# Kernel tuning notes

Hardware: AMD Instinct MI355X
Metric: run time of the kernel (lower is better)

The kernel has to match this reference:

```python
import jax, jax.numpy as jnp
import numpy as np

B, N, DIM, H = 2, 2048, 1024, 16
D = DIM // H

def setup_inputs() -> dict:
    key = jax.random.key(0)
    k1, k2 = jax.random.split(key)
    x = jax.random.normal(k1, (B, N, DIM), dtype=jnp.float32)
    w_qkv = jax.random.normal(k2, (3 * DIM, DIM), dtype=jnp.float32) * (DIM ** -0.5)
    return {"x": x, "w_qkv": w_qkv}

def reference(x, w_qkv):
    b, n, dim = x.shape
    h, d = H, dim // H
    # fused QKV projection: torch Linear computes x @ W.T
    qkv = jnp.einsum('bnd,ed->bne', x, w_qkv)  # [B, N, 3*dim]
    q, k, v = jnp.split(qkv, 3, axis=-1)
    to_heads = lambda t: t.reshape(b, n, h, d).transpose(0, 2, 1, 3)  # [B, H, N, D]
    q, k, v = to_heads(q), to_heads(k), to_heads(v)
    dots = jnp.einsum('bhid,bhjd->bhij', q, k) * (d ** -0.5)  # [B, H, N, N]
    attn = jax.nn.softmax(dots, axis=-1)
    out = jnp.einsum('bhij,bhjd->bhid', attn, v)  # [B, H, N, D]
    # faithful to original: (B,H,N,D) -> (B,N,H,D) -> (B, N*H, D)
    return out.transpose(0, 2, 1, 3).reshape(b, n * h, d)
```

## Files before the change

### kernel.cpp

```cpp
#include <hip/hip_runtime.h>

typedef unsigned short u16;
typedef __bf16 bf16x8 __attribute__((ext_vector_type(8)));
typedef float f32x4 __attribute__((ext_vector_type(4)));

#define BATCH 2
#define NSEQ  2048
#define DIMN  1024
#define NH    16
#define DH    64
#define M_    (BATCH * NSEQ)
#define E_    (3 * DIMN)
#define K_    DIMN
#define QKV_BYTES ((size_t)M_ * E_ * sizeof(u16))
#define XB_ELEMS  ((size_t)M_ * K_)
#define WB_ELEMS  ((size_t)E_ * K_)
#define VT_BYTES  ((size_t)BATCH * NH * DH * NSEQ * sizeof(u16))
#define NEED2     (QKV_BYTES + (XB_ELEMS + WB_ELEMS) * sizeof(u16))
#define NEED3     (NEED2 + VT_BYTES)

__device__ __forceinline__ u16 f2bf(float f) {
  union { float f; unsigned u; } v; v.f = f;
  unsigned r = v.u + 0x7fffu + ((v.u >> 16) & 1u);
  return (u16)(r >> 16);
}
__device__ __forceinline__ uint4 pack8(const float4 a, const float4 b) {
  union { u16 h[8]; uint4 q; } p;
  p.h[0] = f2bf(a.x); p.h[1] = f2bf(a.y); p.h[2] = f2bf(a.z); p.h[3] = f2bf(a.w);
  p.h[4] = f2bf(b.x); p.h[5] = f2bf(b.y); p.h[6] = f2bf(b.z); p.h[7] = f2bf(b.w);
  return p.q;
}
__device__ __forceinline__ void async16(const void* g, void* lds) {
  __builtin_amdgcn_global_load_lds(
      (const __attribute__((address_space(1))) void*)g,
      (__attribute__((address_space(3))) void*)lds, 16, 0, 0);
}
__device__ __forceinline__ unsigned cvtpk_bf16(float lo, float hi) {
  unsigned r;
  asm("v_cvt_pk_bf16_f32 %0, %1, %2" : "=v"(r) : "v"(lo), "v"(hi));
  return r;
}

__global__ __launch_bounds__(256, 4)
void convert_bf16(const float* __restrict__ X, const float* __restrict__ W,
                  u16* __restrict__ Xb, u16* __restrict__ Wb) {
  const size_t nx = XB_ELEMS / 8, nw = WB_ELEMS / 8;
  const size_t stride = (size_t)gridDim.x * blockDim.x;
  for (size_t i = blockIdx.x * blockDim.x + threadIdx.x; i < nx; i += stride) {
    const float4 a = *(const float4*)&X[i * 8];
    const float4 b = *(const float4*)&X[i * 8 + 4];
    *(uint4*)&Xb[i * 8] = pack8(a, b);
  }
  for (size_t i = blockIdx.x * blockDim.x + threadIdx.x; i < nw; i += stride) {
    const float4 a = *(const float4*)&W[i * 8];
    const float4 b = *(const float4*)&W[i * 8 + 4];
    *(uint4*)&Wb[i * 8] = pack8(a, b);
  }
}

__global__ __launch_bounds__(256, 2)
void qkv_gemm_a(const u16* __restrict__ Xb, const u16* __restrict__ Wb,
                u16* __restrict__ QKV, u16* __restrict__ VTg) {
  __shared__ __align__(16) u16 As[128 * 64];
  __shared__ __align__(16) u16 Bs[128 * 64];
  const int tid  = threadIdx.x;
  const int wave = tid >> 6, lane = tid & 63;
  const int m0 = blockIdx.x * 128;
  const int n0 = blockIdx.y * 128;
  const int wm = (wave >> 1) * 64;
  const int wn = (wave & 1) * 64;
  const int lcol = lane & 15, lrow = lane >> 4;
  const int lr8 = lane >> 3;
  const int slog = (lane & 7) ^ lr8;

  f32x4 acc[4][4] = {};

  for (int k0 = 0; k0 < K_; k0 += 64) {
    __syncthreads();
    #pragma unroll
    for (int i = 0; i < 4; ++i) {
      const int g = wave * 4 + i;
      const int r = g * 8 + lr8;
      async16(Xb + (size_t)(m0 + r) * K_ + k0 + slog * 8, &As[g * 512]);
      async16(Wb + (size_t)(n0 + r) * K_ + k0 + slog * 8, &Bs[g * 512]);
    }
    __syncthreads();
    #pragma unroll
    for (int ks = 0; ks < 64; ks += 32) {
      const int segl = (ks >> 3) + lrow;
      bf16x8 af[4], bfr[4];
      #pragma unroll
      for (int i = 0; i < 4; ++i) {
        const int r = wm + lcol + 16 * i;
        af[i] = *(const bf16x8*)&As[r * 64 + ((segl ^ (r & 7)) * 8)];
      }
      #pragma unroll
      for (int j = 0; j < 4; ++j) {
        const int r = wn + lcol + 16 * j;
        bfr[j] = *(const bf16x8*)&Bs[r * 64 + ((segl ^ (r & 7)) * 8)];
      }
      #pragma unroll
      for (int i = 0; i < 4; ++i)
        #pragma unroll
        for (int j = 0; j < 4; ++j)
          acc[i][j] = __builtin_amdgcn_mfma_f32_16x16x32_bf16(
              af[i], bfr[j], acc[i][j], 0, 0, 0);
    }
  }

  if (n0 >= 2 * DIMN) {
    #pragma unroll
    for (int i = 0; i < 4; ++i)
      #pragma unroll
      for (int j = 0; j < 4; ++j) {
        const int gm = m0 + wm + 16 * i + lrow * 4;
        const int bb = gm >> 11, n = gm & (NSEQ - 1);
        const int f = (n0 - 2 * DIMN) + wn + 16 * j + lcol;
        const int h = f >> 6, dd = f & (DH - 1);
        union { u16 h4[4]; uint2 q; } pk;
        #pragma unroll
        for (int r = 0; r < 4; ++r) pk.h4[r] = f2bf(acc[i][j][r]);
        *(uint2*)&VTg[(((size_t)bb * NH + h) * DH + dd) * NSEQ + n] = pk.q;
      }
  } else {
    #pragma unroll
    for (int i = 0; i < 4; ++i)
      #pragma unroll
      for (int j = 0; j < 4; ++j)
        #pragma unroll
        for (int r = 0; r < 4; ++r) {
          const int gm = m0 + wm + 16 * i + lrow * 4 + r;
          const int gn = n0 + wn + 16 * j + lcol;
          QKV[(size_t)gm * E_ + gn] = f2bf(acc[i][j][r]);
        }
  }
}

__global__ __launch_bounds__(256, 2)
void qkv_gemm_f(const float* __restrict__ X, const float* __restrict__ W,
                u16* __restrict__ QKV) {
  __shared__ __align__(16) u16 As[128 * 64];
  __shared__ __align__(16) u16 Bs[128 * 64];
  const int tid  = threadIdx.x;
  const int wave = tid >> 6, lane = tid & 63;
  const int m0 = blockIdx.x * 128, n0 = blockIdx.y * 128;
  const int wm = (wave >> 1) * 64, wn = (wave & 1) * 64;
  const int lcol = lane & 15, lrow = lane >> 4;
  f32x4 acc[4][4] = {};
  for (int k0 = 0; k0 < K_; k0 += 64) {
    __syncthreads();
    #pragma unroll
    for (int p = 0; p < 4; ++p) {
      const int linear = p * 256 + tid;
      const int r = linear >> 3, s = linear & 7;
      const float4 a0 = *(const float4*)&X[(size_t)(m0 + r) * K_ + k0 + s * 8];
      const float4 a1 = *(const float4*)&X[(size_t)(m0 + r) * K_ + k0 + s * 8 + 4];
      const float4 b0 = *(const float4*)&W[(size_t)(n0 + r) * K_ + k0 + s * 8];
      const float4 b1 = *(const float4*)&W[(size_t)(n0 + r) * K_ + k0 + s * 8 + 4];
      const int ph = (s ^ (r & 7)) * 8;
      *(uint4*)&As[r * 64 + ph] = pack8(a0, a1);
      *(uint4*)&Bs[r * 64 + ph] = pack8(b0, b1);
    }
    __syncthreads();
    #pragma unroll
    for (int ks = 0; ks < 64; ks += 32) {
      const int segl = (ks >> 3) + lrow;
      bf16x8 af[4], bfr[4];
      #pragma unroll
      for (int i = 0; i < 4; ++i) {
        const int r = wm + lcol + 16 * i;
        af[i] = *(const bf16x8*)&As[r * 64 + ((segl ^ (r & 7)) * 8)];
      }
      #pragma unroll
      for (int j = 0; j < 4; ++j) {
        const int r = wn + lcol + 16 * j;
        bfr[j] = *(const bf16x8*)&Bs[r * 64 + ((segl ^ (r & 7)) * 8)];
      }
      #pragma unroll
      for (int i = 0; i < 4; ++i)
        #pragma unroll
        for (int j = 0; j < 4; ++j)
          acc[i][j] = __builtin_amdgcn_mfma_f32_16x16x32_bf16(
              af[i], bfr[j], acc[i][j], 0, 0, 0);
    }
  }
  #pragma unroll
  for (int i = 0; i < 4; ++i)
    #pragma unroll
    for (int j = 0; j < 4; ++j)
      #pragma unroll
      for (int r = 0; r < 4; ++r) {
        const int gm = m0 + wm + 16 * i + lrow * 4 + r;
        const int gn = n0 + wn + 16 * j + lcol;
        QKV[(size_t)gm * E_ + gn] = f2bf(acc[i][j][r]);
      }
}

__global__ __launch_bounds__(256, 2)
void attn2(const u16* __restrict__ QKV, const u16* __restrict__ VTg,
           float* __restrict__ Out) {
  __shared__ __align__(16) u16 Ks[64 * 72];
  __shared__ __align__(16) u16 Vs[64 * 72];

  const int tid = threadIdx.x, wave = tid >> 6, lane = tid & 63;
  const int b = blockIdx.x >> 4, h = blockIdx.x & 15;
  const int i0 = blockIdx.y * 128;
  const int lcol = lane & 15, lrow = lane >> 4;
  const size_t base = (size_t)b * NSEQ;
  const int qoff = h * DH, koff = DIMN + h * DH;
  const size_t vbh = ((size_t)b * NH + h) * DH;
  const int sr = tid >> 3;
  const int sg = tid & 7;

  bf16x8 ones;
  #pragma unroll
  for (int t = 0; t < 8; ++t) ones[t] = (__bf16)1.0f;

  bf16x8 aq[2][2];
  #pragma unroll
  for (int qi = 0; qi < 2; ++qi)
    #pragma unroll
    for (int ksi = 0; ksi < 2; ++ksi) {
      const int row = i0 + wave * 32 + qi * 16 + lcol;
      aq[qi][ksi] = *(const bf16x8*)&QKV[(base + row) * E_ + qoff +
                                         (ksi * 4 + lrow) * 8];
    }

  uint4 kreg[2], vreg[2];
  #pragma unroll
  for (int p = 0; p < 2; ++p) {
    const int row = p * 32 + sr;
    kreg[p] = *(const uint4*)&QKV[(base + row) * E_ + koff + sg * 8];
    vreg[p] = *(const uint4*)&VTg[(vbh + row) * NSEQ + sg * 8];
  }

  f32x4 o[2][4] = {};
  f32x4 lacc[2] = {};

  for (int j0 = 0; j0 < NSEQ; j0 += 64) {
    __syncthreads();
    #pragma unroll
    for (int p = 0; p < 2; ++p) {
      const int row = p * 32 + sr;
      *(uint4*)&Ks[row * 72 + sg * 8] = kreg[p];
      *(uint4*)&Vs[row * 72 + sg * 8] = vreg[p];
    }
    __syncthreads();

    if (j0 + 64 < NSEQ) {
      #pragma unroll
      for (int p = 0; p < 2; ++p) {
        const int row = p * 32 + sr;
        kreg[p] = *(const uint4*)&QKV[(base + j0 + 64 + row) * E_ + koff + sg * 8];
        vreg[p] = *(const uint4*)&VTg[(vbh + row) * NSEQ + j0 + 64 + sg * 8];
      }
    }

    f32x4 s2[2][4] = {};
    #pragma unroll
    for (int ksi = 0; ksi < 2; ++ksi) {
      const int seg = ksi * 4 + lrow;
      #pragma unroll
      for (int jt = 0; jt < 4; ++jt) {
        const bf16x8 bk = *(const bf16x8*)&Ks[(jt * 16 + lcol) * 72 + seg * 8];
        #pragma unroll
        for (int qi = 0; qi < 2; ++qi)
          s2[qi][jt] = __builtin_amdgcn_mfma_f32_16x16x32_bf16(
              bk, aq[qi][ksi], s2[qi][jt], 0, 0, 0);
      }
    }

    unsigned apw[2][2][4];
    #pragma unroll
    for (int qi = 0; qi < 2; ++qi) {
      unsigned dw[4][2];
      #pragma unroll
      for (int jt = 0; jt < 4; ++jt) {
        float p[4];
        #pragma unroll
        for (int r = 0; r < 4; ++r)
          p[r] = exp2f(fmaf(s2[qi][jt][r], 0.180336880f, -17.3123405f));
        dw[jt][0] = cvtpk_bf16(p[0], p[1]);
        dw[jt][1] = cvtpk_bf16(p[2], p[3]);
      }
      #pragma unroll
      for (int ksi = 0; ksi < 2; ++ksi)
        #pragma unroll
        for (int u = 0; u < 2; ++u) {
          unsigned x  = dw[2 * ksi][u];
          unsigned x2 = dw[2 * ksi + 1][u];
          asm("v_permlane32_swap_b32 %0, %1" : "+v"(x), "+v"(x2));
          asm("v_permlane16_swap_b32 %0, %1" : "+v"(x), "+v"(x2));
          apw[qi][ksi][u]     = x;
          apw[qi][ksi][2 + u] = x2;
        }
    }

    #pragma unroll
    for (int ksi = 0; ksi < 2; ++ksi) {
      const int seg = ksi * 4 + lrow;
      bf16x8 ap[2];
      #pragma unroll
      for (int qi = 0; qi < 2; ++qi) {
        union { unsigned u[4]; bf16x8 v; } c;
        #pragma unroll
        for (int w = 0; w < 4; ++w) c.u[w] = apw[qi][ksi][w];
        ap[qi] = c.v;
      }
      #pragma unroll
      for (int dt = 0; dt < 4; ++dt) {
        const bf16x8 bv = *(const bf16x8*)&Vs[(dt * 16 + lcol) * 72 + seg * 8];
        #pragma unroll
        for (int qi = 0; qi < 2; ++qi)
          o[qi][dt] = __builtin_amdgcn_mfma_f32_16x16x32_bf16(
              ap[qi], bv, o[qi][dt], 0, 0, 0);
      }
      #pragma unroll
      for (int qi = 0; qi < 2; ++qi)
        lacc[qi] = __builtin_amdgcn_mfma_f32_16x16x32_bf16(
            ap[qi], ones, lacc[qi], 0, 0, 0);
    }
  }

  #pragma unroll
  for (int qi = 0; qi < 2; ++qi)
    #pragma unroll
    for (int r = 0; r < 4; ++r) {
      const float inv = 1.0f / lacc[qi][r];
      const int i = i0 + wave * 32 + qi * 16 + lrow * 4 + r;
      #pragma unroll
      for (int dt = 0; dt < 4; ++dt) {
        const int d = dt * 16 + lcol;
        Out[((base + i) * NH + h) * DH + d] = o[qi][dt][r] * inv;
      }
    }
}

__global__ __launch_bounds__(256, 2)
void attn(const u16* __restrict__ QKV, float* __restrict__ Out) {
  __shared__ __align__(16) u16 Ks[64 * 72];
  __shared__ __align__(16) u16 Vt[64 * 72];
  __shared__ __align__(16) u16 Ps[4][32 * 72];

  const int tid = threadIdx.x, wave = tid >> 6, lane = tid & 63;
  const int b = blockIdx.x >> 4, h = blockIdx.x & 15;
  const int i0 = blockIdx.y * 128;
  const int lcol = lane & 15, lrow = lane >> 4;
  const size_t base = (size_t)b * NSEQ;
  const int qoff = h * DH, koff = DIMN + h * DH, voff = 2 * DIMN + h * DH;
  const int sr = tid >> 3;
  const int sg = tid & 7;

  bf16x8 ones;
  #pragma unroll
  for (int t = 0; t < 8; ++t) ones[t] = (__bf16)1.0f;

  bf16x8 aq[2][2];
  #pragma unroll
  for (int qi = 0; qi < 2; ++qi)
    #pragma unroll
    for (int ksi = 0; ksi < 2; ++ksi) {
      const int row = i0 + wave * 32 + qi * 16 + lcol;
      aq[qi][ksi] = *(const bf16x8*)&QKV[(base + row) * E_ + qoff +
                                         (ksi * 4 + lrow) * 8];
    }

  uint4 kreg[2], vreg[2];
  #pragma unroll
  for (int p = 0; p < 2; ++p) {
    const int row = p * 32 + sr;
    const u16* src = &QKV[(base + row) * E_];
    kreg[p] = *(const uint4*)&src[koff + sg * 8];
    vreg[p] = *(const uint4*)&src[voff + sg * 8];
  }

  f32x4 o[2][4] = {};
  f32x4 lacc[2] = {};

  for (int j0 = 0; j0 < NSEQ; j0 += 64) {
    __syncthreads();
    #pragma unroll
    for (int p = 0; p < 2; ++p) {
      const int row = p * 32 + sr;
      *(uint4*)&Ks[row * 72 + sg * 8] = kreg[p];
      const u16* pv = (const u16*)&vreg[p];
      const int jseg = (row >> 3) & 7, jlo = row & 7;
      #pragma unroll
      for (int t = 0; t < 8; ++t)
        Vt[(sg * 8 + t) * 72 + (((jseg ^ sg) & 7) * 8 + jlo)] = pv[t];
    }
    __syncthreads();

    if (j0 + 64 < NSEQ) {
      #pragma unroll
      for (int p = 0; p < 2; ++p) {
        const int row = p * 32 + sr;
        const u16* src = &QKV[(base + j0 + 64 + row) * E_];
        kreg[p] = *(const uint4*)&src[koff + sg * 8];
        vreg[p] = *(const uint4*)&src[voff + sg * 8];
      }
    }

    f32x4 s[2][4] = {};
    #pragma unroll
    for (int ksi = 0; ksi < 2; ++ksi) {
      const int seg = ksi * 4 + lrow;
      #pragma unroll
      for (int jt = 0; jt < 4; ++jt) {
        const bf16x8 bk = *(const bf16x8*)&Ks[(jt * 16 + lcol) * 72 + seg * 8];
        #pragma unroll
        for (int qi = 0; qi < 2; ++qi)
          s[qi][jt] = __builtin_amdgcn_mfma_f32_16x16x32_bf16(
              aq[qi][ksi], bk, s[qi][jt], 0, 0, 0);
      }
    }

    #pragma unroll
    for (int qi = 0; qi < 2; ++qi)
      #pragma unroll
      for (int jt = 0; jt < 4; ++jt)
        #pragma unroll
        for (int r = 0; r < 4; ++r) {
          const float p = __expf(fmaf(s[qi][jt][r], 0.125f, -12.0f));
          Ps[wave][(qi * 16 + lrow * 4 + r) * 72 + jt * 16 + lcol] = f2bf(p);
        }

    #pragma unroll
    for (int ksi = 0; ksi < 2; ++ksi) {
      const int seg = ksi * 4 + lrow;
      bf16x8 ap[2];
      #pragma unroll
      for (int qi = 0; qi < 2; ++qi)
        ap[qi] = *(const bf16x8*)&Ps[wave][(qi * 16 + lcol) * 72 + seg * 8];
      #pragma unroll
      for (int dt = 0; dt < 4; ++dt) {
        const int d = dt * 16 + lcol;
        const bf16x8 bv = *(const bf16x8*)&Vt[d * 72 + (((seg ^ (d >> 3)) & 7) * 8)];
        #pragma unroll
        for (int qi = 0; qi < 2; ++qi)
          o[qi][dt] = __builtin_amdgcn_mfma_f32_16x16x32_bf16(
              ap[qi], bv, o[qi][dt], 0, 0, 0);
      }
      #pragma unroll
      for (int qi = 0; qi < 2; ++qi)
        lacc[qi] = __builtin_amdgcn_mfma_f32_16x16x32_bf16(
            ap[qi], ones, lacc[qi], 0, 0, 0);
    }
  }

  #pragma unroll
  for (int qi = 0; qi < 2; ++qi)
    #pragma unroll
    for (int r = 0; r < 4; ++r) {
      const float inv = 1.0f / lacc[qi][r];
      const int i = i0 + wave * 32 + qi * 16 + lrow * 4 + r;
      #pragma unroll
      for (int dt = 0; dt < 4; ++dt) {
        const int d = dt * 16 + lcol;
        Out[((base + i) * NH + h) * DH + d] = o[qi][dt][r] * inv;
      }
    }
}

extern "C" void kernel_launch(void* const* d_in, const int* in_sizes, int n_in,
                              void* d_out, int out_size, void* d_ws, size_t ws_size,
                              hipStream_t stream) {
  const float* x = (const float*)d_in[0];
  const float* w = (const float*)d_in[1];
  u16* qkv = (u16*)d_ws;
  float* out = (float*)d_out;

  if (ws_size < QKV_BYTES) return;

  if (ws_size >= NEED3) {
    u16* Xb  = (u16*)((char*)d_ws + QKV_BYTES);
    u16* Wb  = Xb + XB_ELEMS;
    u16* VTg = Wb + WB_ELEMS;
    convert_bf16<<<1024, 256, 0, stream>>>(x, w, Xb, Wb);
    qkv_gemm_a<<<dim3(M_ / 128, E_ / 128), 256, 0, stream>>>(Xb, Wb, qkv, VTg);
    attn2<<<dim3(BATCH * NH, NSEQ / 128), 256, 0, stream>>>(qkv, VTg, out);
  } else {
    qkv_gemm_f<<<dim3(M_ / 128, E_ / 128), 256, 0, stream>>>(x, w, qkv);
    attn<<<dim3(BATCH * NH, NSEQ / 128), 256, 0, stream>>>(qkv, out);
  }
}
```

Baseline: 208.0 us.

## Remap GEMM tiles for XCD locality and stage attention probabilities through LDS

The QKV GEMM now remaps its linear block index so that consecutive blocks on the same XCD share M/N tile neighborhoods, aiming for better L2 reuse. In attention, the permlane-swap register shuffle that laid out the probability tile is replaced by a per-wave swizzled LDS staging buffer, written with software bf16 rounding and read back as MFMA A-operands. s_setprio is raised around the MFMA sections to favor matrix issue. This adds LDS traffic and extra shared memory per block, which may reduce occupancy, and the software rounding costs more ALU than the packed convert instruction.

```diff
diff --git a/kernel.cpp b/kernel.cpp
--- a/kernel.cpp
+++ b/kernel.cpp
@@ -35,11 +35,6 @@
       (const __attribute__((address_space(1))) void*)g,
       (__attribute__((address_space(3))) void*)lds, 16, 0, 0);
 }
-__device__ __forceinline__ unsigned cvtpk_bf16(float lo, float hi) {
-  unsigned r;
-  asm("v_cvt_pk_bf16_f32 %0, %1, %2" : "=v"(r) : "v"(lo), "v"(hi));
-  return r;
-}
 
 __global__ __launch_bounds__(256, 4)
 void convert_bf16(const float* __restrict__ X, const float* __restrict__ W,
@@ -65,8 +60,10 @@
   __shared__ __align__(16) u16 Bs[128 * 64];
   const int tid  = threadIdx.x;
   const int wave = tid >> 6, lane = tid & 63;
-  const int m0 = blockIdx.x * 128;
-  const int n0 = blockIdx.y * 128;
+  const int lin = blockIdx.y * gridDim.x + blockIdx.x;
+  const int nl  = (lin & 7) * 96 + (lin >> 3);
+  const int m0 = (nl & 31) * 128;
+  const int n0 = (nl >> 5) * 128;
   const int wm = (wave >> 1) * 64;
   const int wn = (wave & 1) * 64;
   const int lcol = lane & 15, lrow = lane >> 4;
@@ -197,10 +194,11 @@
 }
 
 __global__ __launch_bounds__(256, 2)
-void attn2(const u16* __restrict__ QKV, const u16* __restrict__ VTg,
+void attn3(const u16* __restrict__ QKV, const u16* __restrict__ VTg,
            float* __restrict__ Out) {
   __shared__ __align__(16) u16 Ks[64 * 72];
   __shared__ __align__(16) u16 Vs[64 * 72];
+  __shared__ __align__(16) u16 Ps[4][32 * 72];
 
   const int tid = threadIdx.x, wave = tid >> 6, lane = tid & 63;
   const int b = blockIdx.x >> 4, h = blockIdx.x & 15;
@@ -211,6 +209,8 @@
   const size_t vbh = ((size_t)b * NH + h) * DH;
   const int sr = tid >> 3;
   const int sg = tid & 7;
+  const int pxor = (lcol & 7) << 4;
+  char* const psw = (char*)&Ps[wave][0];
 
   bf16x8 ones;
   #pragma unroll
@@ -257,6 +257,7 @@
     }
 
     f32x4 s2[2][4] = {};
+    __builtin_amdgcn_s_setprio(1);
     #pragma unroll
     for (int ksi = 0; ksi < 2; ++ksi) {
       const int seg = ksi * 4 + lrow;
@@ -269,31 +270,20 @@
               bk, aq[qi][ksi], s2[qi][jt], 0, 0, 0);
       }
     }
-
-    unsigned apw[2][2][4];
+    __builtin_amdgcn_s_setprio(0);
+
     #pragma unroll
     for (int qi = 0; qi < 2; ++qi) {
-      unsigned dw[4][2];
+      const int rowb = (qi * 16 + lcol) * 144;
       #pragma unroll
       for (int jt = 0; jt < 4; ++jt) {
-        float p[4];
+        union { u16 h4[4]; uint2 q; } pk;
         #pragma unroll
         for (int r = 0; r < 4; ++r)
-          p[r] = exp2f(fmaf(s2[qi][jt][r], 0.180336880f, -17.3123405f));
-        dw[jt][0] = cvtpk_bf16(p[0], p[1]);
-        dw[jt][1] = cvtpk_bf16(p[2], p[3]);
-      }
-      #pragma unroll
-      for (int ksi = 0; ksi < 2; ++ksi)
-        #pragma unroll
-        for (int u = 0; u < 2; ++u) {
-          unsigned x  = dw[2 * ksi][u];
-          unsigned x2 = dw[2 * ksi + 1][u];
-          asm("v_permlane32_swap_b32 %0, %1" : "+v"(x), "+v"(x2));
-          asm("v_permlane16_swap_b32 %0, %1" : "+v"(x), "+v"(x2));
-          apw[qi][ksi][u]     = x;
-          apw[qi][ksi][2 + u] = x2;
-        }
+          pk.h4[r] = f2bf(exp2f(fmaf(s2[qi][jt][r], 0.180336880f, -17.3123405f)));
+        const int jb = (32 * jt + 8 * lrow) ^ pxor;
+        *(uint2*)(psw + rowb + jb) = pk.q;
+      }
     }
 
     #pragma unroll
@@ -301,12 +291,10 @@
       const int seg = ksi * 4 + lrow;
       bf16x8 ap[2];
       #pragma unroll
-      for (int qi = 0; qi < 2; ++qi) {
-        union { unsigned u[4]; bf16x8 v; } c;
-        #pragma unroll
-        for (int w = 0; w < 4; ++w) c.u[w] = apw[qi][ksi][w];
-        ap[qi] = c.v;
-      }
+      for (int qi = 0; qi < 2; ++qi)
+        ap[qi] = *(const bf16x8*)(psw + (qi * 16 + lcol) * 144 +
+                                  ((seg * 16) ^ pxor));
+      __builtin_amdgcn_s_setprio(1);
       #pragma unroll
       for (int dt = 0; dt < 4; ++dt) {
         const bf16x8 bv = *(const bf16x8*)&Vs[(dt * 16 + lcol) * 72 + seg * 8];
@@ -319,6 +307,7 @@
       for (int qi = 0; qi < 2; ++qi)
         lacc[qi] = __builtin_amdgcn_mfma_f32_16x16x32_bf16(
             ap[qi], ones, lacc[qi], 0, 0, 0);
+      __builtin_amdgcn_s_setprio(0);
     }
   }
 
@@ -478,7 +467,7 @@
     u16* VTg = Wb + WB_ELEMS;
     convert_bf16<<<1024, 256, 0, stream>>>(x, w, Xb, Wb);
     qkv_gemm_a<<<dim3(M_ / 128, E_ / 128), 256, 0, stream>>>(Xb, Wb, qkv, VTg);
-    attn2<<<dim3(BATCH * NH, NSEQ / 128), 256, 0, stream>>>(qkv, VTg, out);
+    attn3<<<dim3(BATCH * NH, NSEQ / 128), 256, 0, stream>>>(qkv, VTg, out);
   } else {
     qkv_gemm_f<<<dim3(M_ / 128, E_ / 128), 256, 0, stream>>>(x, w, qkv);
     attn<<<dim3(BATCH * NH, NSEQ / 128), 256, 0, stream>>>(qkv, out);
```

After: 203.1 us. -2.3%, faster.
